# Kernel optimization log

Hardware: AMD Instinct MI355X
Metric: run time of the kernel (lower is better)

## Reference

```python
import jax, jax.numpy as jnp
import numpy as np

NUM_SUBSPACES = 8
CODEBOOK_SIZE = 256
SUBSPACE_DIM = 96


def setup_inputs() -> dict:
    key = jax.random.key(0)
    k1, k2 = jax.random.split(key)
    embeddings = jax.random.normal(k1, (16, 4096, NUM_SUBSPACES * SUBSPACE_DIM), dtype=jnp.float32)
    codebooks = jax.random.normal(k2, (NUM_SUBSPACES, CODEBOOK_SIZE, SUBSPACE_DIM), dtype=jnp.float32)
    return {"embeddings": embeddings, "codebooks": codebooks}


def reference(embeddings, codebooks):
    # embeddings: [B, S, E] with E = M*d; codebooks: [M, K, d]
    B, S, E = embeddings.shape
    M, K, d = codebooks.shape
    # [N, M, d] -> [M, N, d] so each subspace is contiguous
    x = embeddings.reshape(B * S, M, d).transpose(1, 0, 2)
    x2 = jnp.sum(x * x, axis=-1, keepdims=True)              # [M, N, 1]
    c2 = jnp.sum(codebooks * codebooks, axis=-1)[:, None, :]  # [M, 1, K]
    xc = jnp.einsum('mnd,mkd->mnk', x, codebooks)             # [M, N, K]
    dist2 = x2 - 2.0 * xc + c2                                # [M, N, K]
    # argmin over codes (same result as cdist p=2 argmin since sqrt is monotone)
    idx = jnp.argmin(dist2, axis=-1)                          # [M, N]
    # gather nearest codewords per subspace
    quantized = codebooks[jnp.arange(M)[:, None], idx]        # [M, N, d]
    # reassemble: [N, M, d] -> [B, S, E]
    return quantized.transpose(1, 0, 2).reshape(B, S, E)
```

## Files before the change

kernel.cpp:

```cpp
#include <hip/hip_runtime.h>

typedef _Float16 h8 __attribute__((ext_vector_type(8)));
typedef unsigned short u16x8 __attribute__((ext_vector_type(8)));
typedef float   f32x16 __attribute__((ext_vector_type(16)));

constexpr int NSUB  = 8;
constexpr int NCODE = 256;
constexpr int SDIM  = 96;
constexpr int EMB   = NSUB * SDIM;
constexpr float C_SHIFT = 192.0f;
constexpr float THR = 0.04f;

constexpr size_t WS_FRAG_BYTES = (size_t)NSUB * 3072 * 16;
constexpr size_t C2_BYTES      = (size_t)NSUB * NCODE * 4;
constexpr size_t CNT_OFF       = WS_FRAG_BYTES + C2_BYTES;
constexpr size_t LIST_OFF      = CNT_OFF + 16;
constexpr size_t WS_NEEDED     = LIST_OFF + 65536 * 4;

__global__ __launch_bounds__(256) void pq_prep_h(const float* __restrict__ cb,
                                                 unsigned short* __restrict__ wsf,
                                                 float* __restrict__ wsc2)
{
    const int m   = (int)blockIdx.x;
    const int tid = (int)threadIdx.x;
    {
        const float* c = cb + ((size_t)m * NCODE + tid) * SDIM;
        double s = 0.0;
        for (int k = 0; k < SDIM; ++k) { double v = (double)c[k]; s += v * v; }
        wsc2[m * NCODE + tid] = (float)(0.5 * s + (double)C_SHIFT);
    }
    for (int i = 0; i < 12; ++i) {
        int idx = i * 256 + tid;
        int l   = idx & 63;
        int u   = idx >> 6;
        int s   = u % 6;
        int t   = u / 6;
        int code = t * 32 + (l & 31);
        int k0   = s * 16 + (l >> 5) * 8;
        const float* src = cb + (size_t)m * NCODE * SDIM + (size_t)code * SDIM + k0;
        u16x8 o;
        #pragma unroll
        for (int j = 0; j < 8; ++j) {
            _Float16 hv = (_Float16)(-src[j]);
            o[j] = __builtin_bit_cast(unsigned short, hv);
        }
        *(u16x8*)(wsf + ((size_t)m * 3072 + idx) * 8) = o;
    }
}

__global__ __launch_bounds__(128) void pq_mfma20(
    const float* __restrict__ emb,
    const float* __restrict__ cb,
    const unsigned short* __restrict__ wsf,
    const float* __restrict__ wsc2,
    float* __restrict__ out,
    unsigned* __restrict__ gcnt,
    unsigned* __restrict__ glist,
    unsigned cap,
    int nrows,
    int rowblks)
{
    const int tid  = (int)threadIdx.x;
    const int lane = tid & 63;
    const int hib  = lane >> 5;
    const int m    = (int)blockIdx.x & 7;
    const int rb   = ((int)blockIdx.x >> 3) * 2 + (tid >> 6);
    if (rb >= rowblks) return;
    const int row0 = rb * 32;

    const unsigned short* wb = wsf + (size_t)m * 3072 * 8;
    const float* c2p = wsc2 + m * NCODE;

    h8 xh[6];
    {
        int r = row0 + (lane & 31);
        if (r >= nrows) r = nrows - 1;
        const float* xr = emb + (size_t)r * EMB + m * SDIM + hib * 8;
        #pragma unroll
        for (int s = 0; s < 6; ++s) {
            float4 v0 = *(const float4*)(xr + s * 16);
            float4 v1 = *(const float4*)(xr + s * 16 + 4);
            float v[8] = { v0.x, v0.y, v0.z, v0.w, v1.x, v1.y, v1.z, v1.w };
            #pragma unroll
            for (int j = 0; j < 8; ++j) xh[s][j] = (_Float16)v[j];
        }
    }

    float b1 = 3.4e38f, b2 = 3.4e38f;
    int   i1 = 1 << 30;
    #pragma unroll 1
    for (int p = 0; p < 4; ++p) {
        const int t0 = p * 2, t1 = t0 + 1;
        f32x16 a0, a1;
        #pragma unroll
        for (int rq = 0; rq < 4; ++rq) {
            float4 q0 = *(const float4*)(c2p + t0 * 32 + rq * 8 + hib * 4);
            float4 q1 = *(const float4*)(c2p + t1 * 32 + rq * 8 + hib * 4);
            a0[rq*4+0]=q0.x; a0[rq*4+1]=q0.y; a0[rq*4+2]=q0.z; a0[rq*4+3]=q0.w;
            a1[rq*4+0]=q1.x; a1[rq*4+1]=q1.y; a1[rq*4+2]=q1.z; a1[rq*4+3]=q1.w;
        }
        __builtin_amdgcn_s_setprio(1);
        #pragma unroll
        for (int s = 0; s < 6; ++s) {
            h8 c0 = *(const h8*)(wb + (size_t)((t0 * 6 + s) * 64 + lane) * 8);
            h8 c1 = *(const h8*)(wb + (size_t)((t1 * 6 + s) * 64 + lane) * 8);
            a0 = __builtin_amdgcn_mfma_f32_32x32x16_f16(c0, xh[s], a0, 0, 0, 0);
            a1 = __builtin_amdgcn_mfma_f32_32x32x16_f16(c1, xh[s], a1, 0, 0, 0);
        }
        __builtin_amdgcn_s_setprio(0);
        #pragma unroll
        for (int r = 0; r < 16; ++r) {
            float sv = a0[r];
            int   kv = t0 * 32 + (r & 3) + 8 * (r >> 2) + hib * 4;
            if (sv < b1)      { b2 = b1; b1 = sv; i1 = kv; }
            else if (sv < b2) { b2 = sv; }
        }
        #pragma unroll
        for (int r = 0; r < 16; ++r) {
            float sv = a1[r];
            int   kv = t1 * 32 + (r & 3) + 8 * (r >> 2) + hib * 4;
            if (sv < b1)      { b2 = b1; b1 = sv; i1 = kv; }
            else if (sv < b2) { b2 = sv; }
        }
    }
    {
        float ob1 = __shfl_xor(b1, 32);
        int   oi1 = __shfl_xor(i1, 32);
        float ob2 = __shfl_xor(b2, 32);
        bool o_better = (ob1 < b1) || (ob1 == b1 && oi1 < i1);
        float loser = o_better ? b1 : ob1;
        if (o_better) { b1 = ob1; i1 = oi1; }
        b2 = fminf(fminf(b2, ob2), loser);
    }

    {
        int grow = row0 + (lane & 31);
        if (lane < 32 && grow < nrows && (b2 - b1 < THR)) {
            unsigned pos = atomicAdd(gcnt, 1u);
            if (pos < cap) glist[pos] = (unsigned)grow | ((unsigned)m << 20);
        }
    }

    #pragma unroll
    for (int ii = 0; ii < 12; ++ii) {
        int Q = ii * 64 + lane;
        int r = Q / 24, f = Q % 24;
        int grow = row0 + r;
        int k = __shfl(i1, r);
        if (grow < nrows) {
            float4 v = *(const float4*)(cb + ((size_t)m * NCODE + k) * SDIM + f * 4);
            *(float4*)(out + (size_t)grow * EMB + m * SDIM + f * 4) = v;
        }
    }
}

__global__ __launch_bounds__(256) void pq_repair(
    const float* __restrict__ emb,
    const float* __restrict__ cb,
    float* __restrict__ out,
    const unsigned* __restrict__ gcnt,
    const unsigned* __restrict__ glist,
    unsigned cap)
{
    const int tid  = (int)threadIdx.x;
    const int lane = tid & 63;
    const unsigned wv = (unsigned)blockIdx.x * 4u + (unsigned)(tid >> 6);
    unsigned n = *gcnt; if (n > cap) n = cap;
    for (unsigned j = wv; j < n; j += 4096u) {
        unsigned e = glist[j];
        int grow = (int)(e & 0xFFFFFu);
        int m    = (int)(e >> 20);
        const float* xr = emb + (size_t)grow * EMB + m * SDIM;
        double bd = 1e300; int bc = NCODE;
        #pragma unroll 1
        for (int qc = 0; qc < 4; ++qc) {
            int code = qc * 64 + lane;
            const float* cv = cb + ((size_t)m * NCODE + code) * SDIM;
            double acc = 0.0;
            #pragma unroll
            for (int kk = 0; kk < SDIM; kk += 4) {
                float4 xv = *(const float4*)(xr + kk);
                float4 cc = *(const float4*)(cv + kk);
                double d0 = (double)xv.x - (double)cc.x;
                double d1 = (double)xv.y - (double)cc.y;
                double d2 = (double)xv.z - (double)cc.z;
                double d3 = (double)xv.w - (double)cc.w;
                acc += d0*d0 + d1*d1 + d2*d2 + d3*d3;
            }
            if (acc < bd) { bd = acc; bc = code; }
        }
        #pragma unroll
        for (int off = 32; off > 0; off >>= 1) {
            double od = __shfl_xor(bd, off);
            int    oc = __shfl_xor(bc, off);
            if (od < bd || (od == bd && oc < bc)) { bd = od; bc = oc; }
        }
        if (lane < 24) {
            float4 v = *(const float4*)(cb + ((size_t)m * NCODE + bc) * SDIM + lane * 4);
            *(float4*)(out + (size_t)grow * EMB + m * SDIM + lane * 4) = v;
        }
    }
}

__global__ __launch_bounds__(256) void pq_argmin_kernel(
    const float* __restrict__ emb, const float* __restrict__ cb,
    float* __restrict__ out, int nrows)
{
    const int m   = (int)(blockIdx.x & 7);
    const int row = (int)(blockIdx.x >> 3) * 256 + (int)threadIdx.x;
    const float* __restrict__ cbm = cb + (size_t)m * (NCODE * SDIM);
    __shared__ float half_c2[NCODE];
    {
        const int k = (int)threadIdx.x;
        const float* c = cbm + k * SDIM;
        float s = 0.f;
        #pragma unroll
        for (int i = 0; i < SDIM; i += 4) {
            const float4 v = *reinterpret_cast<const float4*>(c + i);
            s = fmaf(v.x, v.x, s); s = fmaf(v.y, v.y, s);
            s = fmaf(v.z, v.z, s); s = fmaf(v.w, v.w, s);
        }
        half_c2[k] = 0.5f * s;
    }
    __syncthreads();
    if (row >= nrows) return;
    float x[SDIM];
    {
        const float* xr = emb + (size_t)row * EMB + m * SDIM;
        #pragma unroll
        for (int i = 0; i < SDIM; i += 4) {
            const float4 v = *reinterpret_cast<const float4*>(xr + i);
            x[i+0] = v.x; x[i+1] = v.y; x[i+2] = v.z; x[i+3] = v.w;
        }
    }
    float best = 3.4e38f, best2 = 3.4e38f;
    int bestk = 0, bestk2 = 0;
    #pragma unroll 1
    for (int k = 0; k < NCODE; k += 4) {
        const float* c0 = cbm + (k + 0) * SDIM;
        const float* c1 = cbm + (k + 1) * SDIM;
        const float* c2 = cbm + (k + 2) * SDIM;
        const float* c3 = cbm + (k + 3) * SDIM;
        float a0 = 0.f, a1 = 0.f, a2 = 0.f, a3 = 0.f;
        #pragma unroll
        for (int i = 0; i < SDIM; i += 4) {
            const float4 v0 = *reinterpret_cast<const float4*>(c0 + i);
            const float4 v1 = *reinterpret_cast<const float4*>(c1 + i);
            const float4 v2 = *reinterpret_cast<const float4*>(c2 + i);
            const float4 v3 = *reinterpret_cast<const float4*>(c3 + i);
            a0 = fmaf(x[i+0], v0.x, a0); a0 = fmaf(x[i+1], v0.y, a0);
            a0 = fmaf(x[i+2], v0.z, a0); a0 = fmaf(x[i+3], v0.w, a0);
            a1 = fmaf(x[i+0], v1.x, a1); a1 = fmaf(x[i+1], v1.y, a1);
            a1 = fmaf(x[i+2], v1.z, a1); a1 = fmaf(x[i+3], v1.w, a1);
            a2 = fmaf(x[i+0], v2.x, a2); a2 = fmaf(x[i+1], v2.y, a2);
            a2 = fmaf(x[i+2], v2.z, a2); a2 = fmaf(x[i+3], v2.w, a2);
            a3 = fmaf(x[i+0], v3.x, a3); a3 = fmaf(x[i+1], v3.y, a3);
            a3 = fmaf(x[i+2], v3.z, a3); a3 = fmaf(x[i+3], v3.w, a3);
        }
        const float s[4] = { half_c2[k+0] - a0, half_c2[k+1] - a1,
                             half_c2[k+2] - a2, half_c2[k+3] - a3 };
        #pragma unroll
        for (int j = 0; j < 4; ++j) {
            if (s[j] < best)       { best2 = best; bestk2 = bestk; best = s[j]; bestk = k + j; }
            else if (s[j] < best2) { best2 = s[j]; bestk2 = k + j; }
        }
    }
    if (best2 - best < 0.02f) {
        const float* ca = cbm + bestk  * SDIM;
        const float* cbv = cbm + bestk2 * SDIM;
        double da = 0.0, db = 0.0;
        for (int i = 0; i < SDIM; ++i) {
            const double ea = (double)x[i] - (double)ca[i];
            const double eb = (double)x[i] - (double)cbv[i];
            da += ea * ea; db += eb * eb;
        }
        if (db < da || (db == da && bestk2 < bestk)) bestk = bestk2;
    }
    const float* cbest = cbm + bestk * SDIM;
    float* o = out + (size_t)row * EMB + m * SDIM;
    #pragma unroll
    for (int i = 0; i < SDIM; i += 4)
        *reinterpret_cast<float4*>(o + i) = *reinterpret_cast<const float4*>(cbest + i);
}

extern "C" void kernel_launch(void* const* d_in, const int* in_sizes, int n_in,
                              void* d_out, int out_size, void* d_ws, size_t ws_size,
                              hipStream_t stream) {
    const float* emb = (const float*)d_in[0];
    const float* cb  = (const float*)d_in[1];
    float* out = (float*)d_out;
    const int nrows = in_sizes[0] / EMB;

    if (ws_size < WS_NEEDED) {
        const int rowBlocks = (nrows + 255) / 256;
        pq_argmin_kernel<<<dim3(rowBlocks * NSUB), dim3(256), 0, stream>>>(emb, cb, out, nrows);
        return;
    }

    unsigned short* wsf = (unsigned short*)d_ws;
    float*    wsc2  = (float*)((char*)d_ws + WS_FRAG_BYTES);
    unsigned* gcnt  = (unsigned*)((char*)d_ws + CNT_OFF);
    unsigned* glist = (unsigned*)((char*)d_ws + LIST_OFF);
    unsigned  cap   = (unsigned)((ws_size - LIST_OFF) / 4);

    hipMemsetAsync(gcnt, 0, 4, stream);
    pq_prep_h<<<dim3(NSUB), dim3(256), 0, stream>>>(cb, wsf, wsc2);

    const int rowblks = (nrows + 31) / 32;
    const int nb      = ((rowblks + 1) / 2) * NSUB;
    pq_mfma20<<<dim3(nb), dim3(128), 0, stream>>>(emb, cb, wsf, wsc2, out,
                                                  gcnt, glist, cap, nrows, rowblks);
    pq_repair<<<dim3(1024), dim3(256), 0, stream>>>(emb, cb, out, gcnt, glist, cap);
}
```

Baseline: 228.4 us.

## Lower near-tie threshold and restructure repair kernel to split dimensions across lanes

Lowers the ambiguity threshold that decides which rows are sent to the exact fp64 repair pass, so fewer rows get flagged. The repair kernel is rewritten so each half-wave handles one code at a time, with lanes splitting the 96 dimensions and reducing through shuffles. Previously each lane looped over whole code vectors with strided loads. This gives coalesced codebook reads and loads x only once, but adds a shuffle reduction per code and leaves 8 of every 32 lanes idle. A smaller threshold risks missing some near-ties that the fp16 MFMA pass gets wrong.

```diff
diff --git a/kernel.cpp b/kernel.cpp
--- a/kernel.cpp
+++ b/kernel.cpp
@@ -9,7 +9,7 @@
 constexpr int SDIM  = 96;
 constexpr int EMB   = NSUB * SDIM;
 constexpr float C_SHIFT = 192.0f;
-constexpr float THR = 0.04f;
+constexpr float THR = 0.03f;
 
 constexpr size_t WS_FRAG_BYTES = (size_t)NSUB * 3072 * 16;
 constexpr size_t C2_BYTES      = (size_t)NSUB * NCODE * 4;
@@ -48,7 +48,7 @@
     }
 }
 
-__global__ __launch_bounds__(128) void pq_mfma20(
+__global__ __launch_bounds__(128) void pq_mfma21(
     const float* __restrict__ emb,
     const float* __restrict__ cb,
     const unsigned short* __restrict__ wsf,
@@ -154,7 +154,7 @@
     }
 }
 
-__global__ __launch_bounds__(256) void pq_repair(
+__global__ __launch_bounds__(256) void pq_repair2(
     const float* __restrict__ emb,
     const float* __restrict__ cb,
     float* __restrict__ out,
@@ -164,39 +164,47 @@
 {
     const int tid  = (int)threadIdx.x;
     const int lane = tid & 63;
+    const int hl   = lane & 31;
+    const int hib  = lane >> 5;
+    const int dch  = hl < 24 ? hl : 23;
+    const bool act = hl < 24;
     const unsigned wv = (unsigned)blockIdx.x * 4u + (unsigned)(tid >> 6);
     unsigned n = *gcnt; if (n > cap) n = cap;
+
     for (unsigned j = wv; j < n; j += 4096u) {
         unsigned e = glist[j];
         int grow = (int)(e & 0xFFFFFu);
         int m    = (int)(e >> 20);
-        const float* xr = emb + (size_t)grow * EMB + m * SDIM;
+        const float* xr  = emb + (size_t)grow * EMB + m * SDIM;
+        const float* cbm = cb + (size_t)m * NCODE * SDIM;
+
+        float4 xv = *(const float4*)(xr + dch * 4);
+
         double bd = 1e300; int bc = NCODE;
         #pragma unroll 1
-        for (int qc = 0; qc < 4; ++qc) {
-            int code = qc * 64 + lane;
-            const float* cv = cb + ((size_t)m * NCODE + code) * SDIM;
-            double acc = 0.0;
-            #pragma unroll
-            for (int kk = 0; kk < SDIM; kk += 4) {
-                float4 xv = *(const float4*)(xr + kk);
-                float4 cc = *(const float4*)(cv + kk);
+        for (int c = 0; c < NCODE; c += 2) {
+            const int code = c + hib;
+            float4 cc = *(const float4*)(cbm + (size_t)code * SDIM + dch * 4);
+            double par = 0.0;
+            if (act) {
                 double d0 = (double)xv.x - (double)cc.x;
                 double d1 = (double)xv.y - (double)cc.y;
                 double d2 = (double)xv.z - (double)cc.z;
                 double d3 = (double)xv.w - (double)cc.w;
-                acc += d0*d0 + d1*d1 + d2*d2 + d3*d3;
+                par = d0*d0 + d1*d1 + d2*d2 + d3*d3;
             }
-            if (acc < bd) { bd = acc; bc = code; }
-        }
-        #pragma unroll
-        for (int off = 32; off > 0; off >>= 1) {
-            double od = __shfl_xor(bd, off);
-            int    oc = __shfl_xor(bc, off);
+            #pragma unroll
+            for (int off = 16; off > 0; off >>= 1)
+                par += __shfl_xor(par, off);
+            if (par < bd) { bd = par; bc = code; }
+        }
+        {
+            double od = __shfl_xor(bd, 32);
+            int    oc = __shfl_xor(bc, 32);
             if (od < bd || (od == bd && oc < bc)) { bd = od; bc = oc; }
         }
         if (lane < 24) {
-            float4 v = *(const float4*)(cb + ((size_t)m * NCODE + bc) * SDIM + lane * 4);
+            float4 v = *(const float4*)(cbm + (size_t)bc * SDIM + lane * 4);
             *(float4*)(out + (size_t)grow * EMB + m * SDIM + lane * 4) = v;
         }
     }
@@ -308,7 +316,7 @@
 
     const int rowblks = (nrows + 31) / 32;
     const int nb      = ((rowblks + 1) / 2) * NSUB;
-    pq_mfma20<<<dim3(nb), dim3(128), 0, stream>>>(emb, cb, wsf, wsc2, out,
+    pq_mfma21<<<dim3(nb), dim3(128), 0, stream>>>(emb, cb, wsf, wsc2, out,
                                                   gcnt, glist, cap, nrows, rowblks);
-    pq_repair<<<dim3(1024), dim3(256), 0, stream>>>(emb, cb, out, gcnt, glist, cap);
-}
+    pq_repair2<<<dim3(1024), dim3(256), 0, stream>>>(emb, cb, out, gcnt, glist, cap);
+}
```

Result: slower. 250.8 us (+9.8%).
